# Performance work log

Hardware: AMD Instinct MI355X
Metric: run time of the kernel (lower is better)

Reference implementation:

```python
import jax, jax.numpy as jnp
import numpy as np

N_NODES = 50000
N_EDGES = 600000
IN_CH = 128
HID_CH = 128
OUT_CH = 64
NUM_GRAPHS = 512


def _gcn_conv(x, W, b, src, dst, n):
    # PyG GCNConv (eval): h = D^{-1/2} (A + I) D^{-1/2} (x W) + b
    h = x @ W  # [N, C]
    loop = jnp.arange(n)
    s = jnp.concatenate([src, loop])  # add self-loops
    d = jnp.concatenate([dst, loop])
    deg = jax.ops.segment_sum(jnp.ones_like(d, dtype=h.dtype), d, num_segments=n)
    dinv = jnp.where(deg > 0, jax.lax.rsqrt(deg), 0.0)
    coef = dinv[s] * dinv[d]  # [E+N]
    msg = h[s] * coef[:, None]  # gather + scale
    out = jax.ops.segment_sum(msg, d, num_segments=n)  # scatter-add
    return out + b


def setup_inputs() -> dict:
    key = jax.random.key(0)
    ks = jax.random.split(key, 10)
    x = jax.random.normal(ks[0], (N_NODES, IN_CH), dtype=jnp.float32)
    edge_index = jax.random.randint(ks[1], (2, N_EDGES), 0, N_NODES, dtype=jnp.int64)
    batch = jnp.sort(jax.random.randint(ks[2], (N_NODES,), 0, NUM_GRAPHS, dtype=jnp.int64))
    sc1 = 1.0 / np.sqrt(IN_CH)
    sc2 = 1.0 / np.sqrt(HID_CH)
    W1 = jax.random.uniform(ks[3], (IN_CH, HID_CH), jnp.float32, -sc1, sc1)
    b1 = jnp.zeros((HID_CH,), jnp.float32)
    W2 = jax.random.uniform(ks[4], (HID_CH, HID_CH), jnp.float32, -sc2, sc2)
    b2 = jnp.zeros((HID_CH,), jnp.float32)
    Wlin = jax.random.uniform(ks[5], (HID_CH, OUT_CH), jnp.float32, -sc2, sc2)
    blin = jax.random.uniform(ks[6], (OUT_CH,), jnp.float32, -sc2, sc2)
    return {"x": x, "W1": W1, "b1": b1, "W2": W2, "b2": b2,
            "Wlin": Wlin, "blin": blin, "edge_index": edge_index, "batch": batch}


def reference(x, W1, b1, W2, b2, Wlin, blin, edge_index, batch):
    n = x.shape[0]
    src, dst = edge_index[0], edge_index[1]
    h = jax.nn.relu(_gcn_conv(x, W1, b1, src, dst, n))
    # dropout: identity in eval mode (training=False)
    h = jax.nn.relu(_gcn_conv(h, W2, b2, src, dst, n))
    # global mean pool over graphs
    summed = jax.ops.segment_sum(h, batch, num_segments=NUM_GRAPHS)
    cnt = jax.ops.segment_sum(jnp.ones((n,), h.dtype), batch, num_segments=NUM_GRAPHS)
    pooled = summed / jnp.maximum(cnt, 1.0)[:, None]
    return pooled @ Wlin + blin  # [NUM_GRAPHS, OUT_CH]
```

## Files before the change

kernel.cpp:

```cpp
#include <hip/hip_runtime.h>

#define N_NODES 50000
#define N_EDGES 600000
#define CH 128
#define NUM_GRAPHS 512
#define OUT_CH 64
#define DSH 6
#define DSTRIDE 64
#define NBUCK 782
#define BPAD 1024

typedef unsigned int uint32;
typedef __attribute__((ext_vector_type(8))) short short8;
typedef __attribute__((ext_vector_type(4))) float floatx4;

__device__ __forceinline__ uint32 bfpack(float a, float b) {
    uint32 ua = __builtin_bit_cast(uint32, a);
    uint32 ub = __builtin_bit_cast(uint32, b);
    ua = (ua + 0x7fffu + ((ua >> 16) & 1u)) >> 16;
    ub = (ub + 0x7fffu + ((ub >> 16) & 1u)) >> 16;
    return (ub << 16) | ua;
}
__device__ __forceinline__ unsigned short bfr(float f) {
    uint32 u = __builtin_bit_cast(uint32, f);
    u = (u + 0x7fffu + ((u >> 16) & 1u)) >> 16;
    return (unsigned short)u;
}
__device__ __forceinline__ float bf_lo(uint32 v) {
    return __builtin_bit_cast(float, v << 16);
}
__device__ __forceinline__ float bf_hi(uint32 v) {
    return __builtin_bit_cast(float, v & 0xffff0000u);
}

__global__ void k_prep(const float* __restrict__ W1, const float* __restrict__ W2,
                       unsigned short* __restrict__ W1t, unsigned short* __restrict__ W2t,
                       int* __restrict__ ccnt) {
    int idx = blockIdx.x * 256 + threadIdx.x;
    if (idx < NBUCK * 16) ccnt[idx] = 0;
    if (idx < 32768) {
        int mat = idx >> 14;
        int rem = idx & 16383;
        int k = rem >> 7, c = rem & 127;
        const float* W = mat ? W2 : W1;
        unsigned short* Wt = mat ? W2t : W1t;
        Wt[c * 128 + k] = bfr(W[k * 128 + c]);
    }
}

__global__ void k_bucket(const int* __restrict__ src, const int* __restrict__ dst,
                         int* __restrict__ ccnt, uint32* __restrict__ cbuck) {
    int e = blockIdx.x * 256 + threadIdx.x;
    if (e < N_EDGES) {
        int s = src[e];
        int d = dst[e];
        int b = d >> DSH;
        int p = atomicAdd(&ccnt[b * 16], 1);
        if (p < BPAD) cbuck[b * BPAD + p] = ((uint32)s << DSH) | (uint32)(d & (DSTRIDE - 1));
    }
}

__global__ __launch_bounds__(256) void k_binfill(const int* __restrict__ ccnt,
                                                 const uint32* __restrict__ cbuck,
                                                 int* __restrict__ srcs,
                                                 int* __restrict__ cur) {
    __shared__ int lbin[DSTRIDE * 64];
    __shared__ int lcnt[64];
    int b = blockIdx.x;
    int tid = threadIdx.x;
    if (tid < 64) lcnt[tid] = 0;
    __syncthreads();
    int n = min(ccnt[b * 16], BPAD);
    int node0 = b << DSH;
    for (int i = tid; i < n; i += 256) {
        uint32 v = cbuck[b * BPAD + i];
        int dl = (int)(v & (DSTRIDE - 1));
        int s = (int)(v >> DSH);
        int p = atomicAdd(&lcnt[dl], 1);
        if (p < DSTRIDE) lbin[dl * DSTRIDE + p] = s;
    }
    __syncthreads();
    #pragma unroll
    for (int it = 0; it < 16; ++it) {
        int idx = it * 256 + tid;
        int dl = idx >> DSH;
        if (node0 + dl < N_NODES) srcs[(node0 << DSH) + idx] = lbin[idx];
    }
    if (tid < 64 && node0 + tid < N_NODES) cur[node0 + tid] = min(lcnt[tid], DSTRIDE);
}

template <bool AF32>
__global__ __launch_bounds__(256, 2) void k_gemm(const void* __restrict__ Av,
                                                 const unsigned short* __restrict__ Wt,
                                                 const int* __restrict__ cur,
                                                 unsigned short* __restrict__ outb) {
    __shared__ __align__(16) unsigned short as_[128][136];
    __shared__ __align__(16) unsigned short bs[128][136];
    int tid = threadIdx.x;
    int row0 = blockIdx.x * 128;

    #pragma unroll
    for (int it = 0; it < 8; ++it) {
        int idx = it * 256 + tid;
        int r = idx >> 4, seg = idx & 15;
        int gr = min(row0 + r, N_NODES - 1);
        if (AF32) {
            const float4* ap = (const float4*)((const float*)Av + (size_t)gr * 128 + seg * 8);
            float4 v0 = ap[0], v1 = ap[1];
            uint4 pk;
            pk.x = bfpack(v0.x, v0.y); pk.y = bfpack(v0.z, v0.w);
            pk.z = bfpack(v1.x, v1.y); pk.w = bfpack(v1.z, v1.w);
            *(uint4*)&as_[r][seg * 8] = pk;
        } else {
            *(uint4*)&as_[r][seg * 8] =
                *(const uint4*)((const unsigned short*)Av + (size_t)gr * 128 + seg * 8);
        }
    }
    #pragma unroll
    for (int it = 0; it < 8; ++it) {
        int idx = it * 256 + tid;
        int c = idx >> 4, seg = idx & 15;
        *(uint4*)&bs[c][seg * 8] = *(const uint4*)&Wt[c * 128 + seg * 8];
    }
    __syncthreads();

    int w = tid >> 6, lane = tid & 63, q = lane >> 4, m = lane & 15;
    int q8 = q * 8;
    floatx4 acc[2][8];
    #pragma unroll
    for (int rt = 0; rt < 2; ++rt)
        #pragma unroll
        for (int ct = 0; ct < 8; ++ct) {
            floatx4 z = {0.f, 0.f, 0.f, 0.f};
            acc[rt][ct] = z;
        }

    #pragma unroll
    for (int kc = 0; kc < 128; kc += 32) {
        short8 a0 = *(const short8*)&as_[w * 32 + m][kc + q8];
        short8 a1 = *(const short8*)&as_[w * 32 + 16 + m][kc + q8];
        #pragma unroll
        for (int ct = 0; ct < 8; ++ct) {
            short8 b = *(const short8*)&bs[ct * 16 + m][kc + q8];
            acc[0][ct] = __builtin_amdgcn_mfma_f32_16x16x32_bf16(a0, b, acc[0][ct], 0, 0, 0);
            acc[1][ct] = __builtin_amdgcn_mfma_f32_16x16x32_bf16(a1, b, acc[1][ct], 0, 0, 0);
        }
    }

    #pragma unroll
    for (int rt = 0; rt < 2; ++rt) {
        #pragma unroll
        for (int i = 0; i < 4; ++i) {
            int gr = row0 + w * 32 + rt * 16 + q * 4 + i;
            if (gr < N_NODES) {
                float sc = rsqrtf((float)(cur[gr] + 1));
                #pragma unroll
                for (int ct = 0; ct < 8; ++ct) {
                    outb[(size_t)gr * 128 + ct * 16 + m] = bfr(acc[rt][ct][i] * sc);
                }
            }
        }
    }
}

template <bool BF16OUT>
__global__ __launch_bounds__(256) void k_agg(const uint32* __restrict__ hb,
                                             const int* __restrict__ cnt_arr,
                                             const int* __restrict__ srcs,
                                             const float* __restrict__ bias,
                                             void* __restrict__ outv) {
    int node = __builtin_amdgcn_readfirstlane(blockIdx.x * 4 + (threadIdx.x >> 6));
    int lane = threadIdx.x & 63;

    int cnt = cnt_arr[node];
    float dn = rsqrtf((float)(cnt + 1));
    uint32 vs = hb[node * 64 + lane];
    float ax = bf_lo(vs), ay = bf_hi(vs);

    int start = node << DSH;
    int last = start + cnt - 1;
    for (int j = 0; j < cnt; j += 8) {
        int i0 = start + j;
        int i1 = min(i0 + 1, last);
        int i2 = min(i0 + 2, last);
        int i3 = min(i0 + 3, last);
        int i4 = min(i0 + 4, last);
        int i5 = min(i0 + 5, last);
        int i6 = min(i0 + 6, last);
        int i7 = min(i0 + 7, last);
        int s0 = srcs[i0], s1 = srcs[i1], s2 = srcs[i2], s3 = srcs[i3];
        int s4 = srcs[i4], s5 = srcs[i5], s6 = srcs[i6], s7 = srcs[i7];
        uint32 v0 = hb[s0 * 64 + lane];
        uint32 v1 = hb[s1 * 64 + lane];
        uint32 v2 = hb[s2 * 64 + lane];
        uint32 v3 = hb[s3 * 64 + lane];
        uint32 v4 = hb[s4 * 64 + lane];
        uint32 v5 = hb[s5 * 64 + lane];
        uint32 v6 = hb[s6 * 64 + lane];
        uint32 v7 = hb[s7 * 64 + lane];
        int rem = cnt - j;
        v1 = (rem > 1) ? v1 : 0u;
        v2 = (rem > 2) ? v2 : 0u;
        v3 = (rem > 3) ? v3 : 0u;
        v4 = (rem > 4) ? v4 : 0u;
        v5 = (rem > 5) ? v5 : 0u;
        v6 = (rem > 6) ? v6 : 0u;
        v7 = (rem > 7) ? v7 : 0u;
        ax += bf_lo(v0); ay += bf_hi(v0);
        ax += bf_lo(v1); ay += bf_hi(v1);
        ax += bf_lo(v2); ay += bf_hi(v2);
        ax += bf_lo(v3); ay += bf_hi(v3);
        ax += bf_lo(v4); ay += bf_hi(v4);
        ax += bf_lo(v5); ay += bf_hi(v5);
        ax += bf_lo(v6); ay += bf_hi(v6);
        ax += bf_lo(v7); ay += bf_hi(v7);
    }
    float2 b = ((const float2*)bias)[lane];
    ax = fmaxf(ax * dn + b.x, 0.f);
    ay = fmaxf(ay * dn + b.y, 0.f);
    if (BF16OUT) ((uint32*)outv)[node * 64 + lane] = bfpack(ax, ay);
    else         ((float2*)outv)[node * 64 + lane] = make_float2(ax, ay);
}

__global__ __launch_bounds__(256) void k_pool_linear(const float* __restrict__ h,
                                                     const int* __restrict__ batch,
                                                     const float* __restrict__ Wl,
                                                     const float* __restrict__ bl,
                                                     float* __restrict__ out) {
    __shared__ int sb[2];
    __shared__ float4 sacc[256];
    __shared__ float xr[CH];
    __shared__ float po[4][OUT_CH];
    int g = blockIdx.x;
    int tid = threadIdx.x;
    if (tid < 2) {
        int target = g + tid;
        int lo = 0, hi = N_NODES;
        while (lo < hi) {
            int mid = (lo + hi) >> 1;
            if (batch[mid] < target) lo = mid + 1; else hi = mid;
        }
        sb[tid] = lo;
    }
    __syncthreads();
    int lo = sb[0], hi = sb[1];
    int q = tid & 31;
    int r = tid >> 5;
    const float4* h4 = (const float4*)h;
    float4 acc = make_float4(0.f, 0.f, 0.f, 0.f);
    for (int i = lo + r; i < hi; i += 8) {
        float4 v = h4[(size_t)i * 32 + q];
        acc.x += v.x; acc.y += v.y; acc.z += v.z; acc.w += v.w;
    }
    sacc[tid] = acc;
    __syncthreads();
    if (r == 0) {
        #pragma unroll
        for (int p = 1; p < 8; ++p) {
            float4 t = sacc[q + p * 32];
            acc.x += t.x; acc.y += t.y; acc.z += t.z; acc.w += t.w;
        }
        float inv = 1.f / (float)((hi - lo) > 0 ? (hi - lo) : 1);
        xr[q * 4 + 0] = acc.x * inv;
        xr[q * 4 + 1] = acc.y * inv;
        xr[q * 4 + 2] = acc.z * inv;
        xr[q * 4 + 3] = acc.w * inv;
    }
    __syncthreads();
    int c = tid & 63;
    int kh = tid >> 6;
    float o = 0.f;
    #pragma unroll 8
    for (int k = kh * 32; k < kh * 32 + 32; ++k) o += xr[k] * Wl[k * OUT_CH + c];
    po[kh][c] = o;
    __syncthreads();
    if (tid < OUT_CH) {
        float v = bl[tid] + po[0][tid] + po[1][tid] + po[2][tid] + po[3][tid];
        out[g * OUT_CH + tid] = v;
    }
}

extern "C" void kernel_launch(void* const* d_in, const int* in_sizes, int n_in,
                              void* d_out, int out_size, void* d_ws, size_t ws_size,
                              hipStream_t stream) {
    const float* x    = (const float*)d_in[0];
    const float* W1   = (const float*)d_in[1];
    const float* b1   = (const float*)d_in[2];
    const float* W2   = (const float*)d_in[3];
    const float* b2   = (const float*)d_in[4];
    const float* Wlin = (const float*)d_in[5];
    const float* blin = (const float*)d_in[6];
    const int* ei     = (const int*)d_in[7];
    const int* batch  = (const int*)d_in[8];
    const int* esrc = ei;
    const int* edst = ei + N_EDGES;
    float* out = (float*)d_out;

    char* w = (char*)d_ws;
    size_t o = 0;
    float* hA            = (float*)(w + o);          o += (size_t)N_NODES * CH * 4;
    unsigned short* hb   = (unsigned short*)(w + o); o += (size_t)N_NODES * CH * 2;
    uint32* habf         = (uint32*)(w + o);         o += (size_t)N_NODES * 64 * 4;
    unsigned short* W1t  = (unsigned short*)(w + o); o += 16384 * 2;
    unsigned short* W2t  = (unsigned short*)(w + o); o += 16384 * 2;
    int* srcs            = (int*)(w + o);            o += (size_t)N_NODES * DSTRIDE * 4;
    int* cur             = (int*)(w + o);            o += (size_t)N_NODES * 4;
    int* ccnt            = (int*)(w + o);            o += (size_t)NBUCK * 16 * 4;
    uint32* cbuck        = (uint32*)(w + o);         o += (size_t)NBUCK * BPAD * 4;
    (void)ws_size; (void)in_sizes; (void)n_in; (void)out_size;

    dim3 b256(256);
    k_prep<<<dim3(128), b256, 0, stream>>>(W1, W2, W1t, W2t, ccnt);
    k_bucket<<<dim3((N_EDGES + 255) / 256), b256, 0, stream>>>(esrc, edst, ccnt, cbuck);
    k_binfill<<<dim3(NBUCK), b256, 0, stream>>>(ccnt, cbuck, srcs, cur);

    dim3 gG((N_NODES + 127) / 128);
    dim3 gA(N_NODES / 4);
    k_gemm<true><<<gG, b256, 0, stream>>>(x, W1t, cur, hb);
    k_agg<true><<<gA, b256, 0, stream>>>((const uint32*)hb, cur, srcs, b1, habf);
    k_gemm<false><<<gG, b256, 0, stream>>>(habf, W2t, cur, hb);
    k_agg<false><<<gA, b256, 0, stream>>>((const uint32*)hb, cur, srcs, b2, hA);
    k_pool_linear<<<dim3(NUM_GRAPHS), b256, 0, stream>>>(hA, batch, Wlin, blin, out);
}
```

Measured before the change: 205.7 us.

## Store GEMM output in channel-sliced layout and aggregate per 16-channel slice

The GEMM now writes its bf16 output as eight channel slices of 16 channels each, so every slice of the whole graph forms a smaller contiguous array. The aggregation kernel launches eight times as many blocks, one per slice. Each wave splits into eight 8-lane groups that gather different neighbours, then combines them with cross-lane shuffles. This is meant to shrink the per-pass gather footprint so it fits in cache better, and to raise memory parallelism for gathers. In exchange, the edge index lists are reread once per slice, 32-byte gathers make poorer use of each transaction, and only one group per wave writes output.

```diff
diff --git a/kernel.cpp b/kernel.cpp
--- a/kernel.cpp
+++ b/kernel.cpp
@@ -156,7 +156,8 @@
                 float sc = rsqrtf((float)(cur[gr] + 1));
                 #pragma unroll
                 for (int ct = 0; ct < 8; ++ct) {
-                    outb[(size_t)gr * 128 + ct * 16 + m] = bfr(acc[rt][ct][i] * sc);
+                    outb[(size_t)ct * (N_NODES * 16) + (size_t)gr * 16 + m] =
+                        bfr(acc[rt][ct][i] * sc);
                 }
             }
         }
@@ -164,62 +165,48 @@
 }
 
 template <bool BF16OUT>
-__global__ __launch_bounds__(256) void k_agg(const uint32* __restrict__ hb,
+__global__ __launch_bounds__(256) void k_agg(const uint32* __restrict__ hbs,
                                              const int* __restrict__ cnt_arr,
                                              const int* __restrict__ srcs,
                                              const float* __restrict__ bias,
                                              void* __restrict__ outv) {
-    int node = __builtin_amdgcn_readfirstlane(blockIdx.x * 4 + (threadIdx.x >> 6));
+    int slice = blockIdx.x & 7;
+    int node = __builtin_amdgcn_readfirstlane(((blockIdx.x >> 3) << 2) + (threadIdx.x >> 6));
     int lane = threadIdx.x & 63;
+    int g = lane >> 3, l = lane & 7;
+    const uint32* base = hbs + (size_t)slice * (N_NODES * 8);
 
     int cnt = cnt_arr[node];
     float dn = rsqrtf((float)(cnt + 1));
-    uint32 vs = hb[node * 64 + lane];
-    float ax = bf_lo(vs), ay = bf_hi(vs);
-
     int start = node << DSH;
-    int last = start + cnt - 1;
-    for (int j = 0; j < cnt; j += 8) {
-        int i0 = start + j;
-        int i1 = min(i0 + 1, last);
-        int i2 = min(i0 + 2, last);
-        int i3 = min(i0 + 3, last);
-        int i4 = min(i0 + 4, last);
-        int i5 = min(i0 + 5, last);
-        int i6 = min(i0 + 6, last);
-        int i7 = min(i0 + 7, last);
-        int s0 = srcs[i0], s1 = srcs[i1], s2 = srcs[i2], s3 = srcs[i3];
-        int s4 = srcs[i4], s5 = srcs[i5], s6 = srcs[i6], s7 = srcs[i7];
-        uint32 v0 = hb[s0 * 64 + lane];
-        uint32 v1 = hb[s1 * 64 + lane];
-        uint32 v2 = hb[s2 * 64 + lane];
-        uint32 v3 = hb[s3 * 64 + lane];
-        uint32 v4 = hb[s4 * 64 + lane];
-        uint32 v5 = hb[s5 * 64 + lane];
-        uint32 v6 = hb[s6 * 64 + lane];
-        uint32 v7 = hb[s7 * 64 + lane];
-        int rem = cnt - j;
-        v1 = (rem > 1) ? v1 : 0u;
-        v2 = (rem > 2) ? v2 : 0u;
-        v3 = (rem > 3) ? v3 : 0u;
-        v4 = (rem > 4) ? v4 : 0u;
-        v5 = (rem > 5) ? v5 : 0u;
-        v6 = (rem > 6) ? v6 : 0u;
-        v7 = (rem > 7) ? v7 : 0u;
+    int last = cnt - 1;
+
+    float ax = 0.f, ay = 0.f;
+    for (int j = 0; j < cnt; j += 16) {
+        int e0 = j + g;
+        int e1 = j + 8 + g;
+        int s0 = srcs[start + min(e0, last)];
+        int s1 = srcs[start + min(e1, last)];
+        uint32 v0 = base[s0 * 8 + l];
+        uint32 v1 = base[s1 * 8 + l];
+        v0 = (e0 < cnt) ? v0 : 0u;
+        v1 = (e1 < cnt) ? v1 : 0u;
         ax += bf_lo(v0); ay += bf_hi(v0);
         ax += bf_lo(v1); ay += bf_hi(v1);
-        ax += bf_lo(v2); ay += bf_hi(v2);
-        ax += bf_lo(v3); ay += bf_hi(v3);
-        ax += bf_lo(v4); ay += bf_hi(v4);
-        ax += bf_lo(v5); ay += bf_hi(v5);
-        ax += bf_lo(v6); ay += bf_hi(v6);
-        ax += bf_lo(v7); ay += bf_hi(v7);
-    }
-    float2 b = ((const float2*)bias)[lane];
+    }
+    ax += __shfl_xor(ax, 8);  ay += __shfl_xor(ay, 8);
+    ax += __shfl_xor(ax, 16); ay += __shfl_xor(ay, 16);
+    ax += __shfl_xor(ax, 32); ay += __shfl_xor(ay, 32);
+    uint32 vs = base[node * 8 + l];
+    ax += bf_lo(vs); ay += bf_hi(vs);
+
+    float2 b = ((const float2*)bias)[slice * 8 + l];
     ax = fmaxf(ax * dn + b.x, 0.f);
     ay = fmaxf(ay * dn + b.y, 0.f);
-    if (BF16OUT) ((uint32*)outv)[node * 64 + lane] = bfpack(ax, ay);
-    else         ((float2*)outv)[node * 64 + lane] = make_float2(ax, ay);
+    if (g == 0) {
+        if (BF16OUT) ((uint32*)outv)[node * 64 + slice * 8 + l] = bfpack(ax, ay);
+        else         ((float2*)outv)[node * 64 + slice * 8 + l] = make_float2(ax, ay);
+    }
 }
 
 __global__ __launch_bounds__(256) void k_pool_linear(const float* __restrict__ h,
@@ -299,7 +286,7 @@
     char* w = (char*)d_ws;
     size_t o = 0;
     float* hA            = (float*)(w + o);          o += (size_t)N_NODES * CH * 4;
-    unsigned short* hb   = (unsigned short*)(w + o); o += (size_t)N_NODES * CH * 2;
+    unsigned short* hbs  = (unsigned short*)(w + o); o += (size_t)N_NODES * CH * 2;
     uint32* habf         = (uint32*)(w + o);         o += (size_t)N_NODES * 64 * 4;
     unsigned short* W1t  = (unsigned short*)(w + o); o += 16384 * 2;
     unsigned short* W2t  = (unsigned short*)(w + o); o += 16384 * 2;
@@ -315,10 +302,10 @@
     k_binfill<<<dim3(NBUCK), b256, 0, stream>>>(ccnt, cbuck, srcs, cur);
 
     dim3 gG((N_NODES + 127) / 128);
-    dim3 gA(N_NODES / 4);
-    k_gemm<true><<<gG, b256, 0, stream>>>(x, W1t, cur, hb);
-    k_agg<true><<<gA, b256, 0, stream>>>((const uint32*)hb, cur, srcs, b1, habf);
-    k_gemm<false><<<gG, b256, 0, stream>>>(habf, W2t, cur, hb);
-    k_agg<false><<<gA, b256, 0, stream>>>((const uint32*)hb, cur, srcs, b2, hA);
+    dim3 gA((N_NODES / 4) * 8);
+    k_gemm<true><<<gG, b256, 0, stream>>>(x, W1t, cur, hbs);
+    k_agg<true><<<gA, b256, 0, stream>>>((const uint32*)hbs, cur, srcs, b1, habf);
+    k_gemm<false><<<gG, b256, 0, stream>>>(habf, W2t, cur, hbs);
+    k_agg<false><<<gA, b256, 0, stream>>>((const uint32*)hbs, cur, srcs, b2, hA);
     k_pool_linear<<<dim3(NUM_GRAPHS), b256, 0, stream>>>(hA, batch, Wlin, blin, out);
 }
```

Measured after the change: 311.3 us. +51.3%, slower.
